# Kernel optimization log

Measured on AMD Instinct MI355X. Metric: run time of the kernel, lower is better.

Reference implementation:

```python
import jax, jax.numpy as jnp
import numpy as np

B, C, H, W = 16, 256, 48, 160
BASELINE = 0.54
REL_ELEV = 1.65
H_MEAN = 1.535


def setup_inputs() -> dict:
    key = jax.random.key(0)
    k = jax.random.split(key, 5)
    features = jax.random.normal(k[0], (B, C, H, W), dtype=jnp.float32)
    # realistic KITTI-style P2 (full-resolution intrinsics; forward divides rows 0:2 by 16)
    base = np.zeros((3, 4), np.float32)
    base[0, 0] = 721.5; base[1, 1] = 721.5
    base[0, 2] = 609.5; base[1, 2] = 172.8
    base[2, 2] = 1.0;   base[1, 3] = 0.2
    P2 = jnp.asarray(base)[None] + 0.5 * jax.random.uniform(k[1], (B, 3, 4), dtype=jnp.float32)
    w_disp = 0.05 * jax.random.normal(k[2], (1, C, 3, 3), dtype=jnp.float32)  # disp_create conv3x3
    b_disp = jnp.zeros((1,), jnp.float32)
    w_ext = 0.05 * jax.random.normal(k[3], (C, C + 1), dtype=jnp.float32)     # extract conv1x1 (O,I)
    b_ext = jnp.zeros((C,), jnp.float32)
    alpha = 0.5 * jnp.ones((1,), jnp.float32)  # nn.Parameter (init 0.0; nonzero to exercise path)
    return {"features": features, "P2": P2, "w_disp": w_disp, "b_disp": b_disp,
            "w_ext": w_ext, "b_ext": b_ext, "alpha": alpha}


def _grid_sample_border(feat, gx, gy):
    """Bilinear grid_sample, padding_mode='border', align_corners=True.
    feat: (B,C1,H,W); gx, gy: (B,H,W) in [-1,1]."""
    Bs, C1, Hs, Ws = feat.shape
    ix = jnp.clip((gx + 1.0) * 0.5 * (Ws - 1), 0.0, Ws - 1)
    iy = jnp.clip((gy + 1.0) * 0.5 * (Hs - 1), 0.0, Hs - 1)
    ix0 = jnp.floor(ix); iy0 = jnp.floor(iy)
    ix1 = jnp.minimum(ix0 + 1.0, Ws - 1); iy1 = jnp.minimum(iy0 + 1.0, Hs - 1)
    wx = (ix - ix0).reshape(Bs, 1, -1)
    wy = (iy - iy0).reshape(Bs, 1, -1)
    flat = feat.reshape(Bs, C1, Hs * Ws)

    def gather(f, yq, xq):
        idx = (yq * Ws + xq).astype(jnp.int32).reshape(-1)
        return f[:, idx]  # (C1, H*W)

    g = jax.vmap(gather)
    v00 = g(flat, iy0, ix0); v01 = g(flat, iy0, ix1)
    v10 = g(flat, iy1, ix0); v11 = g(flat, iy1, ix1)
    out = (v00 * (1 - wx) * (1 - wy) + v01 * wx * (1 - wy)
           + v10 * (1 - wx) * wy + v11 * wx * wy)
    return out.reshape(Bs, C1, Hs, Ws)


def reference(features, P2, w_disp, b_disp, w_ext, b_ext, alpha):
    x = features
    Bs = x.shape[0]
    P2 = P2.at[:, 0:2].set(P2[:, 0:2] / 16.0)
    # disp_create: conv3x3 -> tanh, then detach-scaled
    d = jax.lax.conv_general_dilated(x, w_disp, (1, 1), 'SAME',
                                     dimension_numbers=('NCHW', 'OIHW', 'NCHW'))
    d = jnp.tanh(d + b_disp[None, :, None, None])
    disp = 0.1 * (0.05 * d + 0.95 * jax.lax.stop_gradient(d))  # (B,1,H,W)

    yy = jnp.arange(H, dtype=jnp.float32)[None, :, None]  # (1,H,1): row index
    fy = P2[:, 1:2, 1:2]; cy = P2[:, 1:2, 2:3]; Ty = P2[:, 1:2, 3:4]  # (B,1,1)
    disparity = jax.nn.relu(fy * BASELINE * (yy - cy)
                            / (jnp.abs(fy * REL_ELEV + Ty) + 1e-10))  # (B,H,1)
    disparity = jnp.broadcast_to(disparity, (Bs, H, W))

    x_base = jnp.broadcast_to(jnp.linspace(-1.0, 1.0, W, dtype=jnp.float32)[None, None, :], (Bs, H, W))
    y_base = jnp.linspace(-1.0, 1.0, H, dtype=jnp.float32)[None, :, None]  # (1,H,1)
    y_shifts_base = jax.nn.relu(H_MEAN * (yy - cy) / (2.0 * (REL_ELEV - 0.5 * H_MEAN))) / (H * 0.5)
    y_shifts = y_shifts_base + disp[:, 0]  # (B,H,W)
    gy = y_base + y_shifts

    feats = jnp.concatenate([disparity[:, None], x], axis=1)  # (B,C+1,H,W)
    samp = _grid_sample_border(feats, x_base, gy)
    out = jnp.einsum('oc,bchw->bohw', w_ext, samp) + b_ext[None, :, None, None]
    return jax.nn.relu(x + out * alpha[0])
```

## Files before the change

kernel.cpp:

```cpp
#include <hip/hip_runtime.h>
#include <stdint.h>

#define NB 16
#define NC 256
#define NH 48
#define NW 160
#define HW (NH*NW)
#define NP (NB*HW)

static __device__ __forceinline__ unsigned short f2bf(float f){
  union { float f; uint32_t u; } v; v.f = f;
  uint32_t u = v.u;
  uint32_t r = (u + 0x7FFFu + ((u >> 16) & 1u)) >> 16;
  return (unsigned short)r;
}
static __device__ __forceinline__ float bf2f(unsigned short h){
  union { float f; uint32_t u; } v; v.u = ((uint32_t)h) << 16; return v.f;
}

__global__ __launch_bounds__(256) void kw_conv(const float* __restrict__ w_ext,
                                               const float* __restrict__ w_disp,
                                               unsigned short* __restrict__ WbF,
                                               unsigned short* __restrict__ WtapF){
  int d = blockIdx.x * 256 + threadIdx.x;
  if (blockIdx.x < 256){
    int j  = d & 7;
    int lane = (d >> 3) & 63;
    int mi = (d >> 9) & 3;
    int w  = (d >> 11) & 3;
    int ks = d >> 13;
    int m = w * 64 + mi * 16 + (lane & 15);
    int k = ks * 32 + (lane >> 4) * 8 + j;
    WbF[d] = f2bf(w_ext[m * 257 + 1 + k]);
  } else {
    int d2 = d - 65536;
    int j  = d2 & 7;
    int lane = (d2 >> 3) & 63;
    int ks = d2 >> 9;
    int tap = lane & 15;
    int k = ks * 32 + (lane >> 4) * 8 + j;
    WtapF[d2] = (tap < 9) ? f2bf(w_disp[k * 9 + tap]) : (unsigned short)0;
  }
}

typedef __attribute__((ext_vector_type(8))) short bf16x8;
typedef __attribute__((ext_vector_type(4))) float f32x4;

__global__ __launch_bounds__(256, 2) void kb_gemm(
    const float* __restrict__ x,
    const unsigned short* __restrict__ Wb,
    const unsigned short* __restrict__ Wtap,
    unsigned short* __restrict__ U,
    float* __restrict__ T)
{
  __shared__ __align__(16) unsigned short smem[8 * 2048];
  int bx = blockIdx.x;
  int b  = bx / 120;
  int nt = bx - b * 120;
  int p0 = nt * 64;

  int tid  = threadIdx.x;
  int lane = tid & 63;
  int w    = tid >> 6;
  int l15 = lane & 15;
  int lq  = lane >> 4;

  int q  = tid & 31;
  int cg = tid >> 5;
  const float* xs = x + ((size_t)b * NC + (size_t)cg * 32) * HW + p0 + 2 * q;

  float2 v[32];
  #pragma unroll
  for (int i = 0; i < 32; ++i)
    v[i] = *(const float2*)(xs + (size_t)i * HW);

  bf16x8 afA[4], afB[4];
  bf16x8 atA = {0,0,0,0,0,0,0,0}, atB = {0,0,0,0,0,0,0,0};
  #pragma unroll
  for (int mi = 0; mi < 4; ++mi)
    afA[mi] = *(const bf16x8*)(Wb + ((w * 4 + mi) << 9) + lane * 8);
  if (w == 0)
    atA = *(const bf16x8*)(Wtap + lane * 8);

  f32x4 zero = {0.f, 0.f, 0.f, 0.f};
  f32x4 acc[4][4];
  f32x4 acct[4];
  #pragma unroll
  for (int mi = 0; mi < 4; ++mi){
    acct[mi] = zero;
    #pragma unroll
    for (int ni = 0; ni < 4; ++ni) acc[mi][ni] = zero;
  }

  {
    int n0 = 2 * q;
    unsigned short* sw0 = smem + cg * 2048 + (n0 >> 4) * 512;
    int n15a = n0 & 15;
    #pragma unroll
    for (int g = 0; g < 4; ++g){
      unsigned short ha[8], hb[8];
      #pragma unroll
      for (int j = 0; j < 8; ++j){
        ha[j] = f2bf(v[8 * g + j].x);
        hb[j] = f2bf(v[8 * g + j].y);
      }
      *(bf16x8*)(sw0 + (n15a     + g * 16) * 8) = *(bf16x8*)ha;
      *(bf16x8*)(sw0 + (n15a + 1 + g * 16) * 8) = *(bf16x8*)hb;
    }
  }
  __syncthreads();

#define KB_STEP(T_, AFC, AFN, ATC, ATN)                                       \
  {                                                                           \
    constexpr int t_ = (T_);                                                  \
    if (t_ + 1 < 8) {                                                         \
      _Pragma("unroll")                                                       \
      for (int mi = 0; mi < 4; ++mi)                                          \
        AFN[mi] = *(const bf16x8*)(Wb + (((t_ + 1) * 16 + w * 4 + mi) << 9)   \
                                   + lane * 8);                               \
      if (w == 0)                                                             \
        ATN = *(const bf16x8*)(Wtap + ((t_ + 1) << 9) + lane * 8);            \
    }                                                                         \
    bf16x8 bg[4];                                                             \
    _Pragma("unroll")                                                         \
    for (int ni = 0; ni < 4; ++ni)                                            \
      bg[ni] = *(const bf16x8*)(smem + t_ * 2048 + ni * 512 + lane * 8);      \
    _Pragma("unroll")                                                         \
    for (int mi = 0; mi < 4; ++mi)                                            \
      _Pragma("unroll")                                                       \
      for (int ni = 0; ni < 4; ++ni)                                          \
        acc[mi][ni] = __builtin_amdgcn_mfma_f32_16x16x32_bf16(AFC[mi], bg[ni],\
                                                      acc[mi][ni], 0, 0, 0);  \
    if (w == 0) {                                                             \
      _Pragma("unroll")                                                       \
      for (int ni = 0; ni < 4; ++ni)                                          \
        acct[ni] = __builtin_amdgcn_mfma_f32_16x16x32_bf16(ATC, bg[ni],       \
                                                       acct[ni], 0, 0, 0);    \
    }                                                                         \
  }

  KB_STEP(0, afA, afB, atA, atB)
  KB_STEP(1, afB, afA, atB, atA)
  KB_STEP(2, afA, afB, atA, atB)
  KB_STEP(3, afB, afA, atB, atA)
  KB_STEP(4, afA, afB, atA, atB)
  KB_STEP(5, afB, afA, atB, atA)
  KB_STEP(6, afA, afB, atA, atB)
  KB_STEP(7, afB, afA, atB, atA)
#undef KB_STEP

  #pragma unroll
  for (int mi = 0; mi < 4; ++mi){
    #pragma unroll
    for (int ni = 0; ni < 4; ++ni){
      int o = w * 64 + mi * 16 + lq * 4;
      int n = ni * 16 + l15;
      size_t base = ((size_t)(b * NC + o)) * HW + p0 + n;
      #pragma unroll
      for (int r = 0; r < 4; ++r)
        U[base + (size_t)r * HW] = f2bf(acc[mi][ni][r]);
    }
  }
  if (w == 0){
    #pragma unroll
    for (int ni = 0; ni < 4; ++ni){
      int n = ni * 16 + l15;
      #pragma unroll
      for (int r = 0; r < 4; ++r){
        int k = lq * 4 + r;
        if (k < 9)
          T[(size_t)k * NP + (size_t)b * HW + p0 + n] = acct[ni][r];
      }
    }
  }
}

__global__ __launch_bounds__(256) void kp_grid(
    const float* __restrict__ P2, const float* __restrict__ b_disp,
    const float* __restrict__ T, float4* __restrict__ pre)
{
  int p = blockIdx.x * 256 + threadIdx.x;
  int b  = p / HW;
  int hw = p - b * HW;
  int y  = hw / NW;
  int xx = hw - y * NW;

  float d = 0.f;
  #pragma unroll
  for (int ky = 0; ky < 3; ++ky){
    int yy2 = y + ky - 1;
    if (yy2 < 0 || yy2 >= NH) continue;
    #pragma unroll
    for (int kx = 0; kx < 3; ++kx){
      int xx2 = xx + kx - 1;
      if (xx2 < 0 || xx2 >= NW) continue;
      d += T[(size_t)(ky * 3 + kx) * NP + b * HW + yy2 * NW + xx2];
    }
  }
  float th = tanhf(d + b_disp[0]);

  float fy = P2[b * 12 + 5] * 0.0625f;
  float cy = P2[b * 12 + 6] * 0.0625f;
  float Ty = P2[b * 12 + 7] * 0.0625f;

  float ysb   = fmaxf(1.535f * ((float)y - cy) / 1.765f, 0.f) * (1.f / 24.f);
  float ybase = -1.f + (float)y * (2.f / 47.f);
  float gy = ybase + ysb + 0.1f * th;
  float iy = fminf(fmaxf((gy + 1.f) * 0.5f * 47.f, 0.f), 47.f);
  float fiy0 = floorf(iy);
  float wy = iy - fiy0;
  int iy0 = (int)fiy0;
  int iy1 = min(iy0 + 1, 47);

  float inv_den = 1.f / (fabsf(fy * 1.65f + Ty) + 1e-10f);
  float dr0 = fmaxf(fy * 0.54f * ((float)iy0 - cy) * inv_den, 0.f);
  float dr1 = fmaxf(fy * 0.54f * ((float)iy1 - cy) * inv_den, 0.f);
  float dlerp = (1.f - wy) * dr0 + wy * dr1;

  float4 pr;
  pr.x = wy; pr.y = dlerp;
  pr.z = __int_as_float(iy0 * NW + xx);
  pr.w = __int_as_float(iy1 * NW + xx);
  pre[p] = pr;
}

__global__ __launch_bounds__(256) void kc_epilogue(
    const float* __restrict__ x, const float* __restrict__ w_ext,
    const float* __restrict__ b_ext, const float* __restrict__ alpha,
    const unsigned short* __restrict__ U, const float4* __restrict__ pre,
    float* __restrict__ out)
{
  int bx = blockIdx.x;
  int ptile = bx >> 3;
  int cg    = bx & 7;
  int p = ptile * 256 + threadIdx.x;
  int b  = p / HW;
  int hw = p - b * HW;

  float4 pr = pre[p];
  float wy    = pr.x;
  float dlerp = pr.y;
  int off0 = __float_as_int(pr.z);
  int off1 = __float_as_int(pr.w);
  float w1 = 1.f - wy;
  float al = alpha[0];

  size_t base0 = (size_t)(b * NC) * HW;
  const unsigned short* Ub = U + base0;
  const float* xb = x + base0 + hw;
  float* ob = out + base0 + hw;

  int o0 = cg * 32;
  #pragma unroll 4
  for (int o = o0; o < o0 + 32; ++o){
    float u0 = bf2f(Ub[(size_t)o * HW + off0]);
    float u1 = bf2f(Ub[(size_t)o * HW + off1]);
    float val = w1 * u0 + wy * u1 + w_ext[o * 257] * dlerp + b_ext[o];
    float r = xb[(size_t)o * HW] + al * val;
    ob[(size_t)o * HW] = fmaxf(r, 0.f);
  }
}

extern "C" void kernel_launch(void* const* d_in, const int* in_sizes, int n_in,
                              void* d_out, int out_size, void* d_ws, size_t ws_size,
                              hipStream_t stream) {
  const float* features = (const float*)d_in[0];
  const float* P2       = (const float*)d_in[1];
  const float* w_disp   = (const float*)d_in[2];
  const float* b_disp   = (const float*)d_in[3];
  const float* w_ext    = (const float*)d_in[4];
  const float* b_ext    = (const float*)d_in[5];
  const float* alpha    = (const float*)d_in[6];
  float* out = (float*)d_out;

  char* ws = (char*)d_ws;
  const size_t U_bytes   = (size_t)NP * 256 * 2;
  const size_t T_bytes   = (size_t)9 * NP * 4;
  const size_t pre_bytes = (size_t)NP * 16;
  unsigned short* U    = (unsigned short*)ws;
  float*          T    = (float*)(ws + U_bytes);
  float4*         pre  = (float4*)(ws + U_bytes + T_bytes);
  unsigned short* Wb   = (unsigned short*)(ws + U_bytes + T_bytes + pre_bytes);
  unsigned short* Wtap = Wb + 256 * 256;

  hipLaunchKernelGGL(kw_conv,     dim3(272),  dim3(256), 0, stream, w_ext, w_disp, Wb, Wtap);
  hipLaunchKernelGGL(kb_gemm,     dim3(1920), dim3(256), 0, stream, features, Wb, Wtap, U, T);
  hipLaunchKernelGGL(kp_grid,     dim3(480),  dim3(256), 0, stream, P2, b_disp, T, pre);
  hipLaunchKernelGGL(kc_epilogue, dim3(3840), dim3(256), 0, stream,
                     features, w_ext, b_ext, alpha, U, pre, out);
}
```

Baseline: 303.9 us.

## Issue activation loads via inline asm with staged waitcnts and raise occupancy hint

Replaces the compiler-generated global loads of the activation tile with 32 inline-asm global_load_dwordx2 instructions using a scalar base and vector offsets. Each group's bf16 conversion and LDS store then waits only on its own loads through staged s_waitcnt vmcnt, so conversion overlaps the remaining loads. The launch-bounds occupancy hint goes from 2 to 3 blocks per SM, and the Wtap load becomes unconditional. Risks: the vmcnt(5) count for the last group assumes exactly five later in-flight vector loads (4 Wb plus 1 Wtap), which is fragile. The tighter register budget may also cause spills.

```diff
diff --git a/kernel.cpp b/kernel.cpp
--- a/kernel.cpp
+++ b/kernel.cpp
@@ -46,7 +46,7 @@
 typedef __attribute__((ext_vector_type(8))) short bf16x8;
 typedef __attribute__((ext_vector_type(4))) float f32x4;
 
-__global__ __launch_bounds__(256, 2) void kb_gemm(
+__global__ __launch_bounds__(256, 3) void kb_gemm(
     const float* __restrict__ x,
     const unsigned short* __restrict__ Wb,
     const unsigned short* __restrict__ Wtap,
@@ -67,20 +67,25 @@
 
   int q  = tid & 31;
   int cg = tid >> 5;
-  const float* xs = x + ((size_t)b * NC + (size_t)cg * 32) * HW + p0 + 2 * q;
+  const float* xb_u = x + (size_t)b * NC * HW + p0;
+  uint32_t voff0 = ((uint32_t)cg * 32u * (uint32_t)HW + 2u * (uint32_t)q) * 4u;
 
   float2 v[32];
-  #pragma unroll
-  for (int i = 0; i < 32; ++i)
-    v[i] = *(const float2*)(xs + (size_t)i * HW);
+#define GL(i) asm volatile("global_load_dwordx2 %0, %1, %2"                   \
+    : "=v"(v[i])                                                              \
+    : "v"(voff0 + (uint32_t)((i) * HW * 4)), "s"(xb_u) : "memory")
+  GL(0); GL(1); GL(2); GL(3); GL(4); GL(5); GL(6); GL(7);
+  GL(8); GL(9); GL(10); GL(11); GL(12); GL(13); GL(14); GL(15);
+  GL(16); GL(17); GL(18); GL(19); GL(20); GL(21); GL(22); GL(23);
+  GL(24); GL(25); GL(26); GL(27); GL(28); GL(29); GL(30); GL(31);
+#undef GL
 
   bf16x8 afA[4], afB[4];
-  bf16x8 atA = {0,0,0,0,0,0,0,0}, atB = {0,0,0,0,0,0,0,0};
+  bf16x8 atA, atB = {0,0,0,0,0,0,0,0};
   #pragma unroll
   for (int mi = 0; mi < 4; ++mi)
     afA[mi] = *(const bf16x8*)(Wb + ((w * 4 + mi) << 9) + lane * 8);
-  if (w == 0)
-    atA = *(const bf16x8*)(Wtap + lane * 8);
+  atA = *(const bf16x8*)(Wtap + lane * 8);
 
   f32x4 zero = {0.f, 0.f, 0.f, 0.f};
   f32x4 acc[4][4];
@@ -92,23 +97,38 @@
     for (int ni = 0; ni < 4; ++ni) acc[mi][ni] = zero;
   }
 
-  {
-    int n0 = 2 * q;
-    unsigned short* sw0 = smem + cg * 2048 + (n0 >> 4) * 512;
-    int n15a = n0 & 15;
-    #pragma unroll
-    for (int g = 0; g < 4; ++g){
-      unsigned short ha[8], hb[8];
-      #pragma unroll
-      for (int j = 0; j < 8; ++j){
-        ha[j] = f2bf(v[8 * g + j].x);
-        hb[j] = f2bf(v[8 * g + j].y);
-      }
-      *(bf16x8*)(sw0 + (n15a     + g * 16) * 8) = *(bf16x8*)ha;
-      *(bf16x8*)(sw0 + (n15a + 1 + g * 16) * 8) = *(bf16x8*)hb;
-    }
-  }
-  __syncthreads();
+  int n0 = 2 * q;
+  unsigned short* sw0 = smem + cg * 2048 + (n0 >> 4) * 512;
+  int n15a = n0 & 15;
+#define CVT_GROUP(g)                                                          \
+  { unsigned short ha[8], hb[8];                                              \
+    _Pragma("unroll")                                                         \
+    for (int j = 0; j < 8; ++j){                                              \
+      ha[j] = f2bf(v[8 * (g) + j].x);                                         \
+      hb[j] = f2bf(v[8 * (g) + j].y);                                         \
+    }                                                                         \
+    *(bf16x8*)(sw0 + (n15a     + (g) * 16) * 8) = *(bf16x8*)ha;               \
+    *(bf16x8*)(sw0 + (n15a + 1 + (g) * 16) * 8) = *(bf16x8*)hb;               \
+  }
+
+  asm volatile("s_waitcnt vmcnt(24)" ::: "memory");
+  __builtin_amdgcn_sched_barrier(0);
+  CVT_GROUP(0)
+  asm volatile("s_waitcnt vmcnt(16)" ::: "memory");
+  __builtin_amdgcn_sched_barrier(0);
+  CVT_GROUP(1)
+  asm volatile("s_waitcnt vmcnt(8)" ::: "memory");
+  __builtin_amdgcn_sched_barrier(0);
+  CVT_GROUP(2)
+  asm volatile("s_waitcnt vmcnt(5)" ::: "memory");
+  __builtin_amdgcn_sched_barrier(0);
+  CVT_GROUP(3)
+#undef CVT_GROUP
+
+  asm volatile("s_waitcnt lgkmcnt(0)" ::: "memory");
+  __builtin_amdgcn_sched_barrier(0);
+  __builtin_amdgcn_s_barrier();
+  __builtin_amdgcn_sched_barrier(0);
 
 #define KB_STEP(T_, AFC, AFN, ATC, ATN)                                       \
   {                                                                           \
```

After: 319.0 us. 4.9% more time.
